# Kernel tuning notes

Hardware: AMD Instinct MI355X
Metric: run time of the kernel (lower is better)

Reference implementation:

```python
import jax, jax.numpy as jnp
import numpy as np

B, H = 8192, 2048


def setup_inputs() -> dict:
    key = jax.random.key(0)
    ks = jax.random.split(key, 8)
    s = 1.0 / np.sqrt(H)  # keep pre-activations in a sane range
    return {
        "x": jax.random.normal(ks[0], (B, H), dtype=jnp.float32),
        "ht": jax.random.normal(ks[1], (B, H), dtype=jnp.float32),
        "Wz": jax.random.normal(ks[2], (H, H), dtype=jnp.float32) * s,
        "Uz": jax.random.normal(ks[3], (H, H), dtype=jnp.float32) * s,
        "bz": jnp.zeros((H,), dtype=jnp.float32),
        "Wr": jax.random.normal(ks[4], (H, H), dtype=jnp.float32) * s,
        "Ur": jax.random.normal(ks[5], (H, H), dtype=jnp.float32) * s,
        "br": jnp.zeros((H,), dtype=jnp.float32),
        "Wh": jax.random.normal(ks[6], (H, H), dtype=jnp.float32) * s,
        "Uh": jax.random.normal(ks[7], (H, H), dtype=jnp.float32) * s,
        "bh": jnp.zeros((H,), dtype=jnp.float32),
    }


def reference(x, ht, Wz, Uz, bz, Wr, Ur, br, Wh, Uh, bh):
    # Fuse the three input-side GEMMs and the two state-side gate GEMMs.
    xz, xr, xh = jnp.split(x @ jnp.concatenate([Wz, Wr, Wh], axis=1), 3, axis=-1)
    hz, hr = jnp.split(ht @ jnp.concatenate([Uz, Ur], axis=1), 2, axis=-1)
    z = jax.nn.sigmoid(xz + hz + bz)
    r = jax.nn.sigmoid(xr + hr + br)
    h_tilde = jnp.tanh(xh + (r * ht) @ Uh + bh)
    new_state = (1.0 - z) * ht + z * h_tilde
    return new_state
```

## Files before the change

kernel.cpp:

```cpp
#include <hip/hip_runtime.h>
#include <hip/hip_bf16.h>

typedef unsigned short u16;
typedef __attribute__((ext_vector_type(4))) float f32x4;
typedef __attribute__((ext_vector_type(8))) short bf16x8;
typedef __attribute__((ext_vector_type(4))) unsigned short u16x4;

#define HDIM 2048

__device__ __forceinline__ u16 f2bf(float f) {
  union { float f; unsigned u; } v; v.f = f;
  unsigned r = v.u + 0x7FFFu + ((v.u >> 16) & 1u);
  return (u16)(r >> 16);
}
__device__ __forceinline__ float bf2f(u16 h) {
  union { unsigned u; float f; } v; v.u = ((unsigned)h) << 16;
  return v.f;
}
__device__ __forceinline__ void gload_lds16(const u16* g, void* l) {
  __builtin_amdgcn_global_load_lds(
      (const __attribute__((address_space(1))) unsigned*)g,
      (__attribute__((address_space(3))) unsigned*)l, 16, 0, 0);
}
__device__ __forceinline__ f32x4 mfma16(bf16x8 a, bf16x8 b, f32x4 c) {
  return __builtin_amdgcn_mfma_f32_16x16x32_bf16(a, b, c, 0, 0, 0);
}

__global__ __launch_bounds__(256) void cast_bf(const float* __restrict__ x,
                                               const float* __restrict__ ht,
                                               u16* __restrict__ xb,
                                               u16* __restrict__ hb) {
  const int N4 = 8192 * HDIM / 4;
  int idx = blockIdx.x * 256 + threadIdx.x;
  const float* s; u16* d; int i;
  if (idx < N4) { s = x; d = xb; i = idx; }
  else          { s = ht; d = hb; i = idx - N4; }
  f32x4 v = *(const f32x4*)(s + (size_t)i * 4);
  u16x4 o;
  o.x = f2bf(v.x); o.y = f2bf(v.y); o.z = f2bf(v.z); o.w = f2bf(v.w);
  *(u16x4*)(d + (size_t)i * 4) = o;
}

__global__ __launch_bounds__(256) void transpose_cast6(
    const float* __restrict__ Wz, const float* __restrict__ Uz,
    const float* __restrict__ Wr, const float* __restrict__ Ur,
    const float* __restrict__ Wh, const float* __restrict__ Uh,
    u16* __restrict__ bzrt, u16* __restrict__ whuht) {
  __shared__ float tile[32][33];
  int z = blockIdx.z;
  const float* src; u16* dst;
  switch (z) {
    case 0: src = Wz; dst = bzrt; break;
    case 1: src = Uz; dst = bzrt + 2048; break;
    case 2: src = Wr; dst = bzrt + (size_t)2048 * 4096; break;
    case 3: src = Ur; dst = bzrt + (size_t)2048 * 4096 + 2048; break;
    case 4: src = Wh; dst = whuht; break;
    default: src = Uh; dst = whuht + 2048; break;
  }
  int tx = threadIdx.x & 31, ty = threadIdx.x >> 5;
  int n0 = blockIdx.x * 32, k0 = blockIdx.y * 32;
#pragma unroll
  for (int i = 0; i < 32; i += 8)
    tile[ty + i][tx] = src[(size_t)(k0 + ty + i) * HDIM + n0 + tx];
  __syncthreads();
#pragma unroll
  for (int i = 0; i < 32; i += 8)
    dst[(size_t)(n0 + ty + i) * 4096 + k0 + tx] = f2bf(tile[tx][ty + i]);
}

template <int EPI>
__global__ __launch_bounds__(512, 2) void gemm8p(
    const u16* __restrict__ A0g, const u16* __restrict__ A1g,
    const u16* __restrict__ Btg,
    const float* __restrict__ bias0, const float* __restrict__ bias1,
    const float* __restrict__ htp,
    float* zout, u16* __restrict__ o_a, float* o_final)
{
  __shared__ __attribute__((aligned(16))) char lds[131072];
  const int K = 4096, K0 = 2048, NT = 64;
  const int t = threadIdx.x;
  const int lane = t & 63;
  const int w = t >> 6;
  const int wm = w >> 2, wn = w & 3;

  int nwg = gridDim.x;
  int bid = blockIdx.x;
  int swz = (bid & 7) * (nwg >> 3) + (bid >> 3);
  const int m0 = (swz & 31) * 256;
  const int n0 = (swz >> 5) * 256;

  const int rowT = t >> 2;
  const int srcChunk = (t & 3) ^ ((t >> 3) & 3);
  const int dstOff = t * 16;

  const int lrow = lane & 15;
  const int khi_l = lane >> 4;
  const int chunk = khi_l ^ ((lrow >> 1) & 3);
  const int abase = wm * 8192 + lrow * 64 + chunk * 16;
  const int bbase = wn * 4096 + lrow * 64 + chunk * 16;

  f32x4 acc[8][4];
#pragma unroll
  for (int i = 0; i < 8; ++i)
#pragma unroll
    for (int j = 0; j < 4; ++j) acc[i][j] = (f32x4){0.f, 0.f, 0.f, 0.f};

  auto issueHalf = [&](char* bufbase, int kt, int sub) {
    int kbase = kt * 64 + (sub & 1) * 32 + srcChunk * 8;
    char* dst = bufbase + sub * 16384 + dstOff;
    if (sub < 2) {
      const u16* Ap = A0g; int kk = kbase;
      if (kbase >= K0) { Ap = A1g; kk = kbase - K0; }
      gload_lds16(Ap + (size_t)(m0 + rowT) * K0 + kk, dst);
      gload_lds16(Ap + (size_t)(m0 + 128 + rowT) * K0 + kk, dst + 8192);
    } else {
      gload_lds16(Btg + (size_t)(n0 + rowT) * K + kbase, dst);
      gload_lds16(Btg + (size_t)(n0 + 128 + rowT) * K + kbase, dst + 8192);
    }
  };

  issueHalf(lds, 0, 0); issueHalf(lds, 0, 2);
  issueHalf(lds, 0, 1); issueHalf(lds, 0, 3);
  asm volatile("s_waitcnt vmcnt(4)" ::: "memory");
  __builtin_amdgcn_s_barrier();

  bf16x8 Af[8], B0f[2], B1f[2], B2f[2], B3f[2];
  {
    const char* Bklo = lds + 32768;
    B0f[0] = *(const bf16x8*)(Bklo + bbase);
    B0f[1] = *(const bf16x8*)(Bklo + bbase + 1024);
  }

  for (int kt = 0; kt < NT; ++kt) {
    char* curb = lds + (kt & 1) * 65536;
    char* nxtb = lds + (((kt & 1) ^ 1)) * 65536;
    const char* Aklo = curb;
    const char* Akhi = curb + 16384;
    const char* Bklo = curb + 32768;
    const char* Bkhi = curb + 49152;
    const bool pf = (kt + 1 < NT);

    if (pf) issueHalf(nxtb, kt + 1, 0);
#pragma unroll
    for (int mi = 0; mi < 8; ++mi)
      Af[mi] = *(const bf16x8*)(Aklo + abase + mi * 1024);
    B1f[0] = *(const bf16x8*)(Bklo + bbase + 2048);
    B1f[1] = *(const bf16x8*)(Bklo + bbase + 3072);
    __builtin_amdgcn_s_setprio(1);
#pragma unroll
    for (int mi = 0; mi < 8; ++mi) {
      acc[mi][0] = mfma16(Af[mi], B0f[0], acc[mi][0]);
      acc[mi][1] = mfma16(Af[mi], B0f[1], acc[mi][1]);
    }
    __builtin_amdgcn_s_setprio(0);
    if (pf) { asm volatile("s_waitcnt vmcnt(2)" ::: "memory"); }
    else    { asm volatile("s_waitcnt vmcnt(0)" ::: "memory"); }
    __builtin_amdgcn_s_barrier();

    if (pf) issueHalf(nxtb, kt + 1, 2);
    B2f[0] = *(const bf16x8*)(Bkhi + bbase);
    B2f[1] = *(const bf16x8*)(Bkhi + bbase + 1024);
    __builtin_amdgcn_s_setprio(1);
#pragma unroll
    for (int mi = 0; mi < 8; ++mi) {
      acc[mi][2] = mfma16(Af[mi], B1f[0], acc[mi][2]);
      acc[mi][3] = mfma16(Af[mi], B1f[1], acc[mi][3]);
    }
    __builtin_amdgcn_s_setprio(0);
    __builtin_amdgcn_s_barrier();

    if (pf) issueHalf(nxtb, kt + 1, 1);
#pragma unroll
    for (int mi = 0; mi < 8; ++mi)
      Af[mi] = *(const bf16x8*)(Akhi + abase + mi * 1024);
    B3f[0] = *(const bf16x8*)(Bkhi + bbase + 2048);
    B3f[1] = *(const bf16x8*)(Bkhi + bbase + 3072);
    __builtin_amdgcn_s_setprio(1);
#pragma unroll
    for (int mi = 0; mi < 8; ++mi) {
      acc[mi][0] = mfma16(Af[mi], B2f[0], acc[mi][0]);
      acc[mi][1] = mfma16(Af[mi], B2f[1], acc[mi][1]);
    }
    __builtin_amdgcn_s_setprio(0);
    asm volatile("s_waitcnt vmcnt(2)" ::: "memory");
    __builtin_amdgcn_s_barrier();

    if (pf) issueHalf(nxtb, kt + 1, 3);
    if (pf) {
      const char* BkloN = nxtb + 32768;
      B0f[0] = *(const bf16x8*)(BkloN + bbase);
      B0f[1] = *(const bf16x8*)(BkloN + bbase + 1024);
    }
    __builtin_amdgcn_s_setprio(1);
#pragma unroll
    for (int mi = 0; mi < 8; ++mi) {
      acc[mi][2] = mfma16(Af[mi], B3f[0], acc[mi][2]);
      acc[mi][3] = mfma16(Af[mi], B3f[1], acc[mi][3]);
    }
    __builtin_amdgcn_s_setprio(0);
    __builtin_amdgcn_s_barrier();
  }

  const int rbase = (lane >> 4) * 4;
  const int cbase = lane & 15;
#pragma unroll
  for (int mi = 0; mi < 8; ++mi) {
#pragma unroll
    for (int ni = 0; ni < 4; ++ni) {
#pragma unroll
      for (int j = 0; j < 4; ++j) {
        int row = m0 + wm * 128 + mi * 16 + rbase + j;
        int col = n0 + wn * 64 + ni * 16 + cbase;
        float v = acc[mi][ni][j];
        if constexpr (EPI == 1) {
          if (col < HDIM) {
            float zv = 1.f / (1.f + __expf(-(v + bias0[col])));
            zout[(size_t)row * HDIM + col] = zv;
          } else {
            int c = col - HDIM;
            float rv = 1.f / (1.f + __expf(-(v + bias1[c])));
            o_a[(size_t)row * HDIM + c] = f2bf(rv * htp[(size_t)row * HDIM + c]);
          }
        } else {
          float hv = tanhf(v + bias0[col]);
          float zv = zout[(size_t)row * HDIM + col];
          float hold = htp[(size_t)row * HDIM + col];
          o_final[(size_t)row * HDIM + col] = (1.f - zv) * hold + zv * hv;
        }
      }
    }
  }
}

extern "C" void kernel_launch(void* const* d_in, const int* in_sizes, int n_in,
                              void* d_out, int out_size, void* d_ws, size_t ws_size,
                              hipStream_t stream) {
  const float* x  = (const float*)d_in[0];
  const float* ht = (const float*)d_in[1];
  const float* Wz = (const float*)d_in[2];
  const float* Uz = (const float*)d_in[3];
  const float* bz = (const float*)d_in[4];
  const float* Wr = (const float*)d_in[5];
  const float* Ur = (const float*)d_in[6];
  const float* br = (const float*)d_in[7];
  const float* Wh = (const float*)d_in[8];
  const float* Uh = (const float*)d_in[9];
  const float* bh = (const float*)d_in[10];
  float* out = (float*)d_out;

  char* ws = (char*)d_ws;
  u16* xbf   = (u16*)(ws);
  u16* htbf  = (u16*)(ws + (((size_t)32) << 20));
  u16* abf   = (u16*)(ws + (((size_t)64) << 20));
  u16* bzrt  = (u16*)(ws + (((size_t)96) << 20));
  u16* whuht = (u16*)(ws + (((size_t)128) << 20));

  cast_bf<<<dim3(2 * 8192 * HDIM / 4 / 256), 256, 0, stream>>>(x, ht, xbf, htbf);

  transpose_cast6<<<dim3(64, 64, 6), 256, 0, stream>>>(Wz, Uz, Wr, Ur, Wh, Uh,
                                                       bzrt, whuht);

  gemm8p<1><<<dim3(512), 512, 0, stream>>>(xbf, htbf, bzrt,
      bz, br, ht, out, abf, nullptr);

  gemm8p<2><<<dim3(256), 512, 0, stream>>>(xbf, abf, whuht,
      bh, nullptr, ht, out, nullptr, out);
}
```

Baseline: 878.2 us.

## Restructure GEMM k-loop into barrier-gated phases and regroup tile rasterization

The main GEMM loop is reorganized into four uniform phases. Each phase loads its B fragment from LDS, issues the next global-to-LDS prefetch, hits a barrier, waits on lgkmcnt, and then runs a scheduling-fenced block of MFMAs. This replaces the old scheme that kept several B fragment register sets and preloaded the next tile's B, and the vmcnt waits are retimed to the new issue order. Workgroup-to-tile mapping is also rewritten so groups of 8 blocks cover a 4x8 tile patch, aiming for better L2 reuse. The scheme trades some latency hiding for fewer live registers and more predictable scheduling. It adds extra barriers per iteration, and the new template parameter is unused.

```diff
diff --git a/kernel.cpp b/kernel.cpp
--- a/kernel.cpp
+++ b/kernel.cpp
@@ -68,7 +68,7 @@
     dst[(size_t)(n0 + ty + i) * 4096 + k0 + tx] = f2bf(tile[tx][ty + i]);
 }
 
-template <int EPI>
+template <int EPI, int NTN_LOG2>
 __global__ __launch_bounds__(512, 2) void gemm8p(
     const u16* __restrict__ A0g, const u16* __restrict__ A1g,
     const u16* __restrict__ Btg,
@@ -83,11 +83,11 @@
   const int w = t >> 6;
   const int wm = w >> 2, wn = w & 3;
 
-  int nwg = gridDim.x;
   int bid = blockIdx.x;
-  int swz = (bid & 7) * (nwg >> 3) + (bid >> 3);
-  const int m0 = (swz & 31) * 256;
-  const int n0 = (swz >> 5) * 256;
+  int r = bid >> 3;
+  int g = r >> 5, inner = r & 31;
+  const int m0 = ((bid & 7) * 4 + (inner & 3)) * 256;
+  const int n0 = ((g << 3) + (inner >> 2)) * 256;
 
   const int rowT = t >> 2;
   const int srcChunk = (t & 3) ^ ((t >> 3) & 3);
@@ -124,80 +124,84 @@
   asm volatile("s_waitcnt vmcnt(4)" ::: "memory");
   __builtin_amdgcn_s_barrier();
 
-  bf16x8 Af[8], B0f[2], B1f[2], B2f[2], B3f[2];
-  {
-    const char* Bklo = lds + 32768;
-    B0f[0] = *(const bf16x8*)(Bklo + bbase);
-    B0f[1] = *(const bf16x8*)(Bklo + bbase + 1024);
-  }
+  bf16x8 Af[8], Bf[2];
 
   for (int kt = 0; kt < NT; ++kt) {
     char* curb = lds + (kt & 1) * 65536;
-    char* nxtb = lds + (((kt & 1) ^ 1)) * 65536;
+    char* nxtb = lds + ((kt & 1) ^ 1) * 65536;
     const char* Aklo = curb;
     const char* Akhi = curb + 16384;
     const char* Bklo = curb + 32768;
     const char* Bkhi = curb + 49152;
     const bool pf = (kt + 1 < NT);
 
-    if (pf) issueHalf(nxtb, kt + 1, 0);
 #pragma unroll
     for (int mi = 0; mi < 8; ++mi)
       Af[mi] = *(const bf16x8*)(Aklo + abase + mi * 1024);
-    B1f[0] = *(const bf16x8*)(Bklo + bbase + 2048);
-    B1f[1] = *(const bf16x8*)(Bklo + bbase + 3072);
-    __builtin_amdgcn_s_setprio(1);
-#pragma unroll
-    for (int mi = 0; mi < 8; ++mi) {
-      acc[mi][0] = mfma16(Af[mi], B0f[0], acc[mi][0]);
-      acc[mi][1] = mfma16(Af[mi], B0f[1], acc[mi][1]);
-    }
-    __builtin_amdgcn_s_setprio(0);
-    if (pf) { asm volatile("s_waitcnt vmcnt(2)" ::: "memory"); }
+    Bf[0] = *(const bf16x8*)(Bklo + bbase);
+    Bf[1] = *(const bf16x8*)(Bklo + bbase + 1024);
+    if (pf) issueHalf(nxtb, kt + 1, 0);
+    __builtin_amdgcn_s_barrier();
+    asm volatile("s_waitcnt lgkmcnt(0)" ::: "memory");
+    __builtin_amdgcn_sched_barrier(0);
+    __builtin_amdgcn_s_setprio(1);
+#pragma unroll
+    for (int mi = 0; mi < 8; ++mi) {
+      acc[mi][0] = mfma16(Af[mi], Bf[0], acc[mi][0]);
+      acc[mi][1] = mfma16(Af[mi], Bf[1], acc[mi][1]);
+    }
+    __builtin_amdgcn_s_setprio(0);
+    __builtin_amdgcn_s_barrier();
+
+    Bf[0] = *(const bf16x8*)(Bklo + bbase + 2048);
+    Bf[1] = *(const bf16x8*)(Bklo + bbase + 3072);
+    if (pf) issueHalf(nxtb, kt + 1, 2);
+    __builtin_amdgcn_s_barrier();
+    asm volatile("s_waitcnt lgkmcnt(0)" ::: "memory");
+    __builtin_amdgcn_sched_barrier(0);
+    __builtin_amdgcn_s_setprio(1);
+#pragma unroll
+    for (int mi = 0; mi < 8; ++mi) {
+      acc[mi][2] = mfma16(Af[mi], Bf[0], acc[mi][2]);
+      acc[mi][3] = mfma16(Af[mi], Bf[1], acc[mi][3]);
+    }
+    __builtin_amdgcn_s_setprio(0);
+    if (pf) { asm volatile("s_waitcnt vmcnt(4)" ::: "memory"); }
     else    { asm volatile("s_waitcnt vmcnt(0)" ::: "memory"); }
     __builtin_amdgcn_s_barrier();
 
-    if (pf) issueHalf(nxtb, kt + 1, 2);
-    B2f[0] = *(const bf16x8*)(Bkhi + bbase);
-    B2f[1] = *(const bf16x8*)(Bkhi + bbase + 1024);
-    __builtin_amdgcn_s_setprio(1);
-#pragma unroll
-    for (int mi = 0; mi < 8; ++mi) {
-      acc[mi][2] = mfma16(Af[mi], B1f[0], acc[mi][2]);
-      acc[mi][3] = mfma16(Af[mi], B1f[1], acc[mi][3]);
-    }
-    __builtin_amdgcn_s_setprio(0);
-    __builtin_amdgcn_s_barrier();
-
-    if (pf) issueHalf(nxtb, kt + 1, 1);
 #pragma unroll
     for (int mi = 0; mi < 8; ++mi)
       Af[mi] = *(const bf16x8*)(Akhi + abase + mi * 1024);
-    B3f[0] = *(const bf16x8*)(Bkhi + bbase + 2048);
-    B3f[1] = *(const bf16x8*)(Bkhi + bbase + 3072);
-    __builtin_amdgcn_s_setprio(1);
-#pragma unroll
-    for (int mi = 0; mi < 8; ++mi) {
-      acc[mi][0] = mfma16(Af[mi], B2f[0], acc[mi][0]);
-      acc[mi][1] = mfma16(Af[mi], B2f[1], acc[mi][1]);
-    }
-    __builtin_amdgcn_s_setprio(0);
-    asm volatile("s_waitcnt vmcnt(2)" ::: "memory");
-    __builtin_amdgcn_s_barrier();
-
+    Bf[0] = *(const bf16x8*)(Bkhi + bbase);
+    Bf[1] = *(const bf16x8*)(Bkhi + bbase + 1024);
+    if (pf) issueHalf(nxtb, kt + 1, 1);
+    __builtin_amdgcn_s_barrier();
+    asm volatile("s_waitcnt lgkmcnt(0)" ::: "memory");
+    __builtin_amdgcn_sched_barrier(0);
+    __builtin_amdgcn_s_setprio(1);
+#pragma unroll
+    for (int mi = 0; mi < 8; ++mi) {
+      acc[mi][0] = mfma16(Af[mi], Bf[0], acc[mi][0]);
+      acc[mi][1] = mfma16(Af[mi], Bf[1], acc[mi][1]);
+    }
+    __builtin_amdgcn_s_setprio(0);
+    __builtin_amdgcn_s_barrier();
+
+    Bf[0] = *(const bf16x8*)(Bkhi + bbase + 2048);
+    Bf[1] = *(const bf16x8*)(Bkhi + bbase + 3072);
     if (pf) issueHalf(nxtb, kt + 1, 3);
-    if (pf) {
-      const char* BkloN = nxtb + 32768;
-      B0f[0] = *(const bf16x8*)(BkloN + bbase);
-      B0f[1] = *(const bf16x8*)(BkloN + bbase + 1024);
-    }
-    __builtin_amdgcn_s_setprio(1);
-#pragma unroll
-    for (int mi = 0; mi < 8; ++mi) {
-      acc[mi][2] = mfma16(Af[mi], B3f[0], acc[mi][2]);
-      acc[mi][3] = mfma16(Af[mi], B3f[1], acc[mi][3]);
-    }
-    __builtin_amdgcn_s_setprio(0);
+    __builtin_amdgcn_s_barrier();
+    asm volatile("s_waitcnt lgkmcnt(0)" ::: "memory");
+    __builtin_amdgcn_sched_barrier(0);
+    __builtin_amdgcn_s_setprio(1);
+#pragma unroll
+    for (int mi = 0; mi < 8; ++mi) {
+      acc[mi][2] = mfma16(Af[mi], Bf[0], acc[mi][2]);
+      acc[mi][3] = mfma16(Af[mi], Bf[1], acc[mi][3]);
+    }
+    __builtin_amdgcn_s_setprio(0);
+    if (pf) { asm volatile("s_waitcnt vmcnt(4)" ::: "memory"); }
     __builtin_amdgcn_s_barrier();
   }
 
@@ -260,9 +264,9 @@
   transpose_cast6<<<dim3(64, 64, 6), 256, 0, stream>>>(Wz, Uz, Wr, Ur, Wh, Uh,
                                                        bzrt, whuht);
 
-  gemm8p<1><<<dim3(512), 512, 0, stream>>>(xbf, htbf, bzrt,
+  gemm8p<1, 4><<<dim3(512), 512, 0, stream>>>(xbf, htbf, bzrt,
       bz, br, ht, out, abf, nullptr);
 
-  gemm8p<2><<<dim3(256), 512, 0, stream>>>(xbf, abf, whuht,
+  gemm8p<2, 3><<<dim3(256), 512, 0, stream>>>(xbf, abf, whuht,
       bh, nullptr, ht, out, nullptr, out);
 }
```

Result: faster. 756.1 us (-13.9%).
